# Kernel tuning notes

Measured on AMD Instinct MI355X. Metric: run time of the kernel, lower is better.

## Reference

```python
import jax, jax.numpy as jnp
import numpy as np

D = 32          # max_delay_block
NEG_INF = -1e13 # matches module's self.neg_inf


def setup_inputs() -> dict:
    key = jax.random.key(0)
    ks = jax.random.split(key, 8)
    b, c, t, f, h = 2, 128, 512, 64, 32
    xm = jax.random.normal(ks[0], (b, c, t, f), dtype=jnp.float32)
    xf = jax.random.normal(ks[1], (b, c, t, f), dtype=jnp.float32)
    # pointwise_conv1 / pointwise_conv2: 1x1 convs == per-pixel linear maps c->h
    w1 = jax.random.normal(ks[2], (c, h), dtype=jnp.float32) * (1.0 / np.sqrt(c))
    b1 = jax.random.normal(ks[3], (h,), dtype=jnp.float32) * 0.01
    w2 = jax.random.normal(ks[4], (c, h), dtype=jnp.float32) * (1.0 / np.sqrt(c))
    b2 = jax.random.normal(ks[5], (h,), dtype=jnp.float32) * 0.01
    # conv2d: h -> 1 channels, kernel (5,3)   (OIHW layout)
    wc = jax.random.normal(ks[6], (1, h, 5, 3), dtype=jnp.float32) * (1.0 / np.sqrt(h * 15))
    bc = jax.random.normal(ks[7], (1,), dtype=jnp.float32) * 0.01
    return {"xm": xm, "xf": xf, "w1": w1, "b1": b1, "w2": w2, "b2": b2, "wc": wc, "bc": bc}


def reference(xm, xf, w1, b1, w2, b2, wc, bc):
    b, c, t, f = xf.shape
    # 1x1 convs (per time-freq bin linear projections)
    xm1 = jnp.einsum('bctf,ch->bhtf', xm, w1) + b1[None, :, None, None]
    xf1 = jnp.einsum('bctf,ch->bhtf', xf, w2) + b2[None, :, None, None]

    # delay windows: window j at frame i looks at original frame i + j - (D-1)
    # (j = D-1 is zero delay, j = 0 is delay D-1; out-of-range frames are zero-padded)
    idx = jnp.arange(t)[:, None] + jnp.arange(D)[None, :]          # [t, D] into padded time
    xf1p = jnp.pad(xf1, ((0, 0), (0, 0), (D - 1, 0), (0, 0)))      # [b,h,t+D-1,f]
    win = xf1p[:, :, idx, :]                                       # [b,h,t,D,f]
    corr = jnp.einsum('bhtf,bhtdf->bhtd', xm1, win)                # [b,h,t,D]

    # conv2d smoothing: kernel (5,3), pad (3,1) -> height t+2, keep first t rows
    corr1 = jax.lax.conv_general_dilated(
        corr, wc, window_strides=(1, 1), padding=((3, 3), (1, 1)),
        dimension_numbers=('NCHW', 'OIHW', 'NCHW'))
    corr1 = corr1[:, 0, :t, :] + bc[0]                             # [b,t,D]

    # causal mask: frame i cannot attend to delays pointing before frame 0,
    # i.e. positions with i + j < D - 1 get neg_inf (exactly tril().flip() logic)
    bad = (jnp.arange(t)[:, None] + jnp.arange(D)[None, :]) < (D - 1)
    corr1 = jnp.where(bad[None, :, :], NEG_INF, corr1)
    w = jax.nn.softmax(corr1, axis=-1)                             # [b,t,D]

    # delay-weighted sum over the raw far-end features
    xfp = jnp.pad(xf, ((0, 0), (0, 0), (D - 1, 0), (0, 0)))        # [b,c,t+D-1,f]
    win2 = xfp[:, :, idx, :]                                       # [b,c,t,D,f]
    out = jnp.einsum('btd,bctdf->bctf', w, win2)                   # [b,c,t,f]
    return out
```

## Files before the change

### kernel.cpp

```cpp
#include <hip/hip_runtime.h>

typedef unsigned short u16;
typedef unsigned int   u32;

#define B_ 2
#define C_ 128
#define T_ 512
#define F_ 64
#define H_ 32
#define D_ 32

#define XM1_OUT 0u
#define XF1_OUT 2097152u

#define CORR_OFF 0u
#define CORR_N   1127168u
#define WQ_OFF   1127168u
#define WT_OFF   1159936u
#define FLAG_OFF 1168673u

__device__ __forceinline__ float scrub_u(u32 v){
  return ((v & 0x7F800000u) == 0x7F800000u) ? 0.f : __uint_as_float(v);
}
__device__ __forceinline__ float bf_lo(u32 u){ return scrub_u(u << 16); }
__device__ __forceinline__ float bf_hi(u32 u){ return scrub_u(u & 0xffff0000u); }
__device__ __forceinline__ float bf1(u16 v){ return scrub_u(((u32)v) << 16); }
__device__ __forceinline__ float f32s(float x){ return scrub_u(__float_as_uint(x)); }
__device__ __forceinline__ u16 f2bf(float x){
  u32 u = __float_as_uint(x);
  u32 r = u + 0x7fffu + ((u >> 16) & 1u);
  return (u16)(r >> 16);
}

__global__ __launch_bounds__(256) void kd_detect(const u16* __restrict__ w1, u32* __restrict__ flag){
  __shared__ int cnt;
  if (threadIdx.x == 0) cnt = 0;
  __syncthreads();
  int c = 0;
  for (int i = threadIdx.x * 2; i < 4096; i += 512){
    u32 e = ((u32)w1[i] >> 7) & 0xFFu;
    if (e >= 0xBFu) c++;
  }
  atomicAdd(&cnt, c);
  __syncthreads();
  if (threadIdx.x == 0) flag[0] = (cnt > 16) ? 1u : 0u;
}

__global__ __launch_bounds__(256) void k0_init(const void* __restrict__ w1, const void* __restrict__ b1,
                                               const void* __restrict__ w2, const void* __restrict__ b2,
                                               const void* __restrict__ wc, const void* __restrict__ bc,
                                               float* __restrict__ ws, const u32* __restrict__ flag){
  u32 i = blockIdx.x * 256u + threadIdx.x;
  float* cp = ws + CORR_OFF;
  for (u32 k = i; k < CORR_N; k += gridDim.x * 256u) cp[k] = 0.f;
  float* wt = ws + WT_OFF;
  u32 isf = *flag;
  if (!isf){
    const u16* W1=(const u16*)w1; const u16* B1=(const u16*)b1;
    const u16* W2=(const u16*)w2; const u16* B2=(const u16*)b2;
    const u16* WC=(const u16*)wc; const u16* BC=(const u16*)bc;
    if (i < 4096u) wt[i]        = bf1(W1[i]);
    if (i < 32u)   wt[4096u+i]  = bf1(B1[i]);
    if (i < 4096u) wt[4128u+i]  = bf1(W2[i]);
    if (i < 32u)   wt[8224u+i]  = bf1(B2[i]);
    if (i < 480u)  wt[8256u+i]  = bf1(WC[i]);
    if (i == 0u)   wt[8736u]    = bf1(BC[0]);
  } else {
    const float* W1=(const float*)w1; const float* B1=(const float*)b1;
    const float* W2=(const float*)w2; const float* B2=(const float*)b2;
    const float* WC=(const float*)wc; const float* BC=(const float*)bc;
    if (i < 4096u) wt[i]        = f32s(W1[i]);
    if (i < 32u)   wt[4096u+i]  = f32s(B1[i]);
    if (i < 4096u) wt[4128u+i]  = f32s(W2[i]);
    if (i < 32u)   wt[8224u+i]  = f32s(B2[i]);
    if (i < 480u)  wt[8256u+i]  = f32s(WC[i]);
    if (i == 0u)   wt[8736u]    = f32s(BC[0]);
  }
}

__global__ __launch_bounds__(256) void k1_proj(const void* __restrict__ xm, const void* __restrict__ xf,
                                               const float* __restrict__ wt, const u32* __restrict__ flag,
                                               float* __restrict__ xm1, float* __restrict__ xf1){
  int bt  = blockIdx.x >> 6;
  int b   = bt >> 1, sel = bt & 1;
  int m0  = (((blockIdx.x & 63) << 8) + threadIdx.x) * 2;
  const void* Xv = sel ? xf : xm;
  const float* W = wt + (sel ? 4128 : 0);
  const float* bias = wt + (sel ? 8224 : 4096);
  u32 isf = *flag;

  float acc0[H_], acc1[H_];
#pragma unroll
  for (int h = 0; h < H_; h++){ acc0[h] = 0.f; acc1[h] = 0.f; }

  if (!isf){
    const u16* X = (const u16*)Xv + (size_t)b * (C_*T_*F_);
    for (int c = 0; c < C_; c++){
      u32 u = *(const u32*)(X + (size_t)c * (T_*F_) + m0);
      float x0 = bf_lo(u), x1 = bf_hi(u);
#pragma unroll
      for (int h = 0; h < H_; h++){
        float wv = W[c * H_ + h];
        acc0[h] += x0 * wv;
        acc1[h] += x1 * wv;
      }
    }
  } else {
    const float* X = (const float*)Xv + (size_t)b * (C_*T_*F_);
    for (int c = 0; c < C_; c++){
      float2 xv = *(const float2*)(X + (size_t)c * (T_*F_) + m0);
      float x0 = f32s(xv.x), x1 = f32s(xv.y);
#pragma unroll
      for (int h = 0; h < H_; h++){
        float wv = W[c * H_ + h];
        acc0[h] += x0 * wv;
        acc1[h] += x1 * wv;
      }
    }
  }
  float* O = (sel ? xf1 : xm1) + (size_t)b * (H_*T_*F_);
#pragma unroll
  for (int h = 0; h < H_; h++){
    float bv = bias[h];
    *(float2*)(O + (size_t)h * (T_*F_) + m0) = make_float2(acc0[h] + bv, acc1[h] + bv);
  }
}

__global__ __launch_bounds__(256) void k2_corr(const float* __restrict__ xm1, const float* __restrict__ xf1,
                                               float* __restrict__ corr_pad){
  int blk = blockIdx.x;
  int tt = blk & 7, h = (blk >> 3) & 31, b = blk >> 8;
  int t0 = tt * 64;
  const float* A  = xm1 + ((size_t)(b*H_ + h)) * (T_*F_);
  const float* Bm = xf1 + ((size_t)(b*H_ + h)) * (T_*F_);

  __shared__ float Al[64*68];
  __shared__ float Bl[95*68];
  int tid = threadIdx.x;

  for (int idx = tid; idx < 64*16; idx += 256){
    int r = idx >> 4, q = idx & 15;
    *(float4*)(Al + r*68 + q*4) = *(const float4*)(A + (size_t)(t0 + r)*F_ + q*4);
  }
  for (int idx = tid; idx < 95*16; idx += 256){
    int r = idx >> 4, q = idx & 15;
    int gr = t0 - 31 + r;
    float4 v = make_float4(0.f,0.f,0.f,0.f);
    if (gr >= 0) v = *(const float4*)(Bm + (size_t)gr*F_ + q*4);
    *(float4*)(Bl + r*68 + q*4) = v;
  }
  __syncthreads();

  int tl = tid >> 2, dg = tid & 3;
  float acc[8];
#pragma unroll
  for (int j = 0; j < 8; j++) acc[j] = 0.f;

  for (int fq = 0; fq < 16; fq++){
    float4 a = *(const float4*)(Al + tl*68 + fq*4);
#pragma unroll
    for (int j = 0; j < 8; j++){
      float4 bv = *(const float4*)(Bl + (tl + dg*8 + j)*68 + fq*4);
      acc[j] += a.x*bv.x + a.y*bv.y + a.z*bv.z + a.w*bv.w;
    }
  }
  float* o = corr_pad + ((size_t)(b*H_ + h))*(518*34) + (size_t)(t0 + tl + 3)*34 + (dg*8 + 1);
#pragma unroll
  for (int j = 0; j < 8; j++) o[j] = acc[j];
}

__global__ __launch_bounds__(256) void k3_conv_softmax(const float* __restrict__ corr_pad,
                                                       const float* __restrict__ wt,
                                                       float* __restrict__ wq){
  int b  = blockIdx.x >> 6;
  int t0 = (blockIdx.x & 63) * 8;
  int tid = threadIdx.x;
  int tl = tid >> 5, d = tid & 31;
  int t = t0 + tl;

  const float* wcf = wt + 8256;
  float val = wt[8736];
  const float* cp = corr_pad + (size_t)b * (H_*518*34);

  for (int h = 0; h < H_; h++){
    const float* cph = cp + (size_t)h*(518*34) + (size_t)t*34 + d;
    const float* wch = wcf + h*15;
#pragma unroll
    for (int kh = 0; kh < 5; kh++){
#pragma unroll
      for (int kw = 0; kw < 3; kw++){
        val += cph[kh*34 + kw] * wch[kh*3 + kw];
      }
    }
  }
  if (t + d < D_ - 1) val = -1e13f;

  float m = val;
#pragma unroll
  for (int off = 16; off > 0; off >>= 1) m = fmaxf(m, __shfl_xor(m, off));
  float e = __expf(val - m);
  float s = e;
#pragma unroll
  for (int off = 16; off > 0; off >>= 1) s += __shfl_xor(s, off);

  wq[((size_t)b*T_ + t)*D_ + d] = e / s;
}

__global__ __launch_bounds__(256) void k4_out(const void* __restrict__ xf, const float* __restrict__ wq,
                                              const u32* __restrict__ flag, void* __restrict__ out){
  int blk = blockIdx.x;
  int tt = blk & 7, c = (blk >> 3) & 127, b = blk >> 10;
  int t0 = tt * 64;
  u32 isf = *flag;

  __shared__ float xfl[95*68];
  __shared__ float wl[64*33];
  int tid = threadIdx.x;

  if (!isf){
    const u16* Xf = (const u16*)xf + ((size_t)(b*C_ + c)) * (T_*F_);
    for (int idx = tid; idx < 95*16; idx += 256){
      int r = idx >> 4, q = idx & 15;
      int gr = t0 - 31 + r;
      float4 v = make_float4(0.f,0.f,0.f,0.f);
      if (gr >= 0){
        uint2 u = *(const uint2*)(Xf + (size_t)gr*F_ + q*4);
        v.x = bf_lo(u.x); v.y = bf_hi(u.x); v.z = bf_lo(u.y); v.w = bf_hi(u.y);
      }
      *(float4*)(xfl + r*68 + q*4) = v;
    }
  } else {
    const float* Xf = (const float*)xf + ((size_t)(b*C_ + c)) * (T_*F_);
    for (int idx = tid; idx < 95*16; idx += 256){
      int r = idx >> 4, q = idx & 15;
      int gr = t0 - 31 + r;
      float4 v = make_float4(0.f,0.f,0.f,0.f);
      if (gr >= 0){
        float4 u = *(const float4*)(Xf + (size_t)gr*F_ + q*4);
        v.x = f32s(u.x); v.y = f32s(u.y); v.z = f32s(u.z); v.w = f32s(u.w);
      }
      *(float4*)(xfl + r*68 + q*4) = v;
    }
  }
  for (int idx = tid; idx < 64*8; idx += 256){
    int r = idx >> 3, q = idx & 7;
    float4 v = *(const float4*)(wq + ((size_t)b*T_ + t0 + r)*D_ + q*4);
    wl[r*33 + q*4 + 0] = v.x; wl[r*33 + q*4 + 1] = v.y;
    wl[r*33 + q*4 + 2] = v.z; wl[r*33 + q*4 + 3] = v.w;
  }
  __syncthreads();

  int tg = tid >> 4, q = tid & 15;
  float4 acc[4];
#pragma unroll
  for (int j = 0; j < 4; j++) acc[j] = make_float4(0.f,0.f,0.f,0.f);

#pragma unroll
  for (int rr = 0; rr < 35; rr++){
    float4 xv = *(const float4*)(xfl + (tg*4 + rr)*68 + q*4);
#pragma unroll
    for (int j = 0; j < 4; j++){
      int d = rr - j;
      if (d >= 0 && d < D_){
        float wv = wl[(tg*4 + j)*33 + d];
        acc[j].x += wv * xv.x; acc[j].y += wv * xv.y;
        acc[j].z += wv * xv.z; acc[j].w += wv * xv.w;
      }
    }
  }
  if (!isf){
#pragma unroll
    for (int j = 0; j < 4; j++){
      int t = t0 + tg*4 + j;
      u16* O = (u16*)out + (((size_t)(b*C_ + c))*T_ + t)*F_ + q*4;
      u32 lo = (u32)f2bf(acc[j].x) | ((u32)f2bf(acc[j].y) << 16);
      u32 hi = (u32)f2bf(acc[j].z) | ((u32)f2bf(acc[j].w) << 16);
      *(uint2*)O = make_uint2(lo, hi);
    }
  } else {
#pragma unroll
    for (int j = 0; j < 4; j++){
      int t = t0 + tg*4 + j;
      float* O = (float*)out + (((size_t)(b*C_ + c))*T_ + t)*F_ + q*4;
      *(float4*)O = acc[j];
    }
  }
}

extern "C" void kernel_launch(void* const* d_in, const int* in_sizes, int n_in,
                              void* d_out, int out_size, void* d_ws, size_t ws_size,
                              hipStream_t stream) {
  const void* xm = d_in[0];
  const void* xf = d_in[1];
  float* ws = (float*)d_ws;
  u32* flag = (u32*)(ws + FLAG_OFF);

  float* xm1 = (float*)d_out + XM1_OUT;
  float* xf1 = (float*)d_out + XF1_OUT;

  hipLaunchKernelGGL(kd_detect, dim3(1), dim3(256), 0, stream, (const u16*)d_in[2], flag);
  hipLaunchKernelGGL(k0_init, dim3(1024), dim3(256), 0, stream, d_in[2], d_in[3], d_in[4],
                     d_in[5], d_in[6], d_in[7], ws, flag);
  hipLaunchKernelGGL(k1_proj, dim3(256), dim3(256), 0, stream, xm, xf, ws + WT_OFF, flag, xm1, xf1);
  hipLaunchKernelGGL(k2_corr, dim3(512), dim3(256), 0, stream, xm1, xf1, ws + CORR_OFF);
  hipLaunchKernelGGL(k3_conv_softmax, dim3(128), dim3(256), 0, stream, ws + CORR_OFF,
                     ws + WT_OFF, ws + WQ_OFF);
  hipLaunchKernelGGL(k4_out, dim3(2048), dim3(256), 0, stream, xf, ws + WQ_OFF, flag, d_out);
}
```

Baseline: 200.1 us.

## Drop dtype detection and weight-staging kernels, stage inputs through shared memory

Result: faster. 188.0 us (-6.0%).

```diff
diff --git a/kernel.cpp b/kernel.cpp
--- a/kernel.cpp
+++ b/kernel.cpp
@@ -14,116 +14,49 @@
 #define XF1_OUT 2097152u
 
 #define CORR_OFF 0u
-#define CORR_N   1127168u
 #define WQ_OFF   1127168u
-#define WT_OFF   1159936u
-#define FLAG_OFF 1168673u
-
-__device__ __forceinline__ float scrub_u(u32 v){
-  return ((v & 0x7F800000u) == 0x7F800000u) ? 0.f : __uint_as_float(v);
-}
-__device__ __forceinline__ float bf_lo(u32 u){ return scrub_u(u << 16); }
-__device__ __forceinline__ float bf_hi(u32 u){ return scrub_u(u & 0xffff0000u); }
-__device__ __forceinline__ float bf1(u16 v){ return scrub_u(((u32)v) << 16); }
-__device__ __forceinline__ float f32s(float x){ return scrub_u(__float_as_uint(x)); }
-__device__ __forceinline__ u16 f2bf(float x){
-  u32 u = __float_as_uint(x);
-  u32 r = u + 0x7fffu + ((u >> 16) & 1u);
-  return (u16)(r >> 16);
-}
-
-__global__ __launch_bounds__(256) void kd_detect(const u16* __restrict__ w1, u32* __restrict__ flag){
-  __shared__ int cnt;
-  if (threadIdx.x == 0) cnt = 0;
-  __syncthreads();
-  int c = 0;
-  for (int i = threadIdx.x * 2; i < 4096; i += 512){
-    u32 e = ((u32)w1[i] >> 7) & 0xFFu;
-    if (e >= 0xBFu) c++;
-  }
-  atomicAdd(&cnt, c);
-  __syncthreads();
-  if (threadIdx.x == 0) flag[0] = (cnt > 16) ? 1u : 0u;
-}
-
-__global__ __launch_bounds__(256) void k0_init(const void* __restrict__ w1, const void* __restrict__ b1,
-                                               const void* __restrict__ w2, const void* __restrict__ b2,
-                                               const void* __restrict__ wc, const void* __restrict__ bc,
-                                               float* __restrict__ ws, const u32* __restrict__ flag){
-  u32 i = blockIdx.x * 256u + threadIdx.x;
-  float* cp = ws + CORR_OFF;
-  for (u32 k = i; k < CORR_N; k += gridDim.x * 256u) cp[k] = 0.f;
-  float* wt = ws + WT_OFF;
-  u32 isf = *flag;
-  if (!isf){
-    const u16* W1=(const u16*)w1; const u16* B1=(const u16*)b1;
-    const u16* W2=(const u16*)w2; const u16* B2=(const u16*)b2;
-    const u16* WC=(const u16*)wc; const u16* BC=(const u16*)bc;
-    if (i < 4096u) wt[i]        = bf1(W1[i]);
-    if (i < 32u)   wt[4096u+i]  = bf1(B1[i]);
-    if (i < 4096u) wt[4128u+i]  = bf1(W2[i]);
-    if (i < 32u)   wt[8224u+i]  = bf1(B2[i]);
-    if (i < 480u)  wt[8256u+i]  = bf1(WC[i]);
-    if (i == 0u)   wt[8736u]    = bf1(BC[0]);
-  } else {
-    const float* W1=(const float*)w1; const float* B1=(const float*)b1;
-    const float* W2=(const float*)w2; const float* B2=(const float*)b2;
-    const float* WC=(const float*)wc; const float* BC=(const float*)bc;
-    if (i < 4096u) wt[i]        = f32s(W1[i]);
-    if (i < 32u)   wt[4096u+i]  = f32s(B1[i]);
-    if (i < 4096u) wt[4128u+i]  = f32s(W2[i]);
-    if (i < 32u)   wt[8224u+i]  = f32s(B2[i]);
-    if (i < 480u)  wt[8256u+i]  = f32s(WC[i]);
-    if (i == 0u)   wt[8736u]    = f32s(BC[0]);
-  }
-}
-
-__global__ __launch_bounds__(256) void k1_proj(const void* __restrict__ xm, const void* __restrict__ xf,
-                                               const float* __restrict__ wt, const u32* __restrict__ flag,
+
+__global__ __launch_bounds__(256) void k1_proj(const float* __restrict__ xm, const float* __restrict__ xf,
+                                               const float* __restrict__ w1, const float* __restrict__ b1,
+                                               const float* __restrict__ w2, const float* __restrict__ b2,
                                                float* __restrict__ xm1, float* __restrict__ xf1){
-  int bt  = blockIdx.x >> 6;
-  int b   = bt >> 1, sel = bt & 1;
-  int m0  = (((blockIdx.x & 63) << 8) + threadIdx.x) * 2;
-  const void* Xv = sel ? xf : xm;
-  const float* W = wt + (sel ? 4128 : 0);
-  const float* bias = wt + (sel ? 8224 : 4096);
-  u32 isf = *flag;
-
-  float acc0[H_], acc1[H_];
-#pragma unroll
-  for (int h = 0; h < H_; h++){ acc0[h] = 0.f; acc1[h] = 0.f; }
-
-  if (!isf){
-    const u16* X = (const u16*)Xv + (size_t)b * (C_*T_*F_);
-    for (int c = 0; c < C_; c++){
-      u32 u = *(const u32*)(X + (size_t)c * (T_*F_) + m0);
-      float x0 = bf_lo(u), x1 = bf_hi(u);
-#pragma unroll
-      for (int h = 0; h < H_; h++){
-        float wv = W[c * H_ + h];
-        acc0[h] += x0 * wv;
-        acc1[h] += x1 * wv;
-      }
-    }
-  } else {
-    const float* X = (const float*)Xv + (size_t)b * (C_*T_*F_);
-    for (int c = 0; c < C_; c++){
-      float2 xv = *(const float2*)(X + (size_t)c * (T_*F_) + m0);
-      float x0 = f32s(xv.x), x1 = f32s(xv.y);
-#pragma unroll
-      for (int h = 0; h < H_; h++){
-        float wv = W[c * H_ + h];
-        acc0[h] += x0 * wv;
-        acc1[h] += x1 * wv;
-      }
-    }
-  }
-  float* O = (sel ? xf1 : xm1) + (size_t)b * (H_*T_*F_);
-#pragma unroll
-  for (int h = 0; h < H_; h++){
-    float bv = bias[h];
-    *(float2*)(O + (size_t)h * (T_*F_) + m0) = make_float2(acc0[h] + bv, acc1[h] + bv);
-  }
+  int blk  = blockIdx.x;
+  int mblk = blk & 127;
+  int bt   = blk >> 7;
+  int b    = bt >> 1, sel = bt & 1;
+  int tid  = threadIdx.x;
+  int m0   = mblk * 256;
+
+  const float* X    = (sel ? xf : xm) + (size_t)b * (C_*T_*F_);
+  const float* W    = sel ? w2 : w1;
+  const float* bias = sel ? b2 : b1;
+
+  __shared__ float ls[32*256];
+
+  float acc[H_];
+#pragma unroll
+  for (int h = 0; h < H_; h++) acc[h] = 0.f;
+
+  for (int cc = 0; cc < C_; cc += 32){
+    for (int idx = tid; idx < 32*64; idx += 256){
+      int r = idx >> 6, q = idx & 63;
+      *(float4*)(ls + r*256 + q*4) =
+        *(const float4*)(X + (size_t)(cc + r) * (T_*F_) + m0 + q*4);
+    }
+    __syncthreads();
+#pragma unroll
+    for (int r = 0; r < 32; r++){
+      float x = ls[r*256 + tid];
+      const float* Wr = W + (cc + r) * H_;
+#pragma unroll
+      for (int h = 0; h < H_; h++) acc[h] += x * Wr[h];
+    }
+    __syncthreads();
+  }
+
+  float* O = (sel ? xf1 : xm1) + (size_t)b * (H_*T_*F_) + m0 + tid;
+#pragma unroll
+  for (int h = 0; h < H_; h++) O[(size_t)h * (T_*F_)] = acc[h] + bias[h];
 }
 
 __global__ __launch_bounds__(256) void k2_corr(const float* __restrict__ xm1, const float* __restrict__ xf1,
@@ -170,26 +103,35 @@
 }
 
 __global__ __launch_bounds__(256) void k3_conv_softmax(const float* __restrict__ corr_pad,
-                                                       const float* __restrict__ wt,
+                                                       const float* __restrict__ wc, const float* __restrict__ bc,
                                                        float* __restrict__ wq){
   int b  = blockIdx.x >> 6;
   int t0 = (blockIdx.x & 63) * 8;
   int tid = threadIdx.x;
+
+  __shared__ float ls[32*12*34];
+  const float* cp = corr_pad + (size_t)b * (H_*518*34);
+  for (int idx = tid; idx < 32*12*34; idx += 256){
+    int h = idx / 408, rem = idx - h*408;
+    int r = rem / 34, dd = rem - r*34;
+    int gr = t0 + r;
+    bool halo = (gr < 3) | (gr > 514) | (dd == 0) | (dd == 33);
+    ls[idx] = halo ? 0.f : cp[(size_t)h*(518*34) + (size_t)gr*34 + dd];
+  }
+  __syncthreads();
+
   int tl = tid >> 5, d = tid & 31;
   int t = t0 + tl;
 
-  const float* wcf = wt + 8256;
-  float val = wt[8736];
-  const float* cp = corr_pad + (size_t)b * (H_*518*34);
-
+  float val = bc[0];
   for (int h = 0; h < H_; h++){
-    const float* cph = cp + (size_t)h*(518*34) + (size_t)t*34 + d;
-    const float* wch = wcf + h*15;
+    const float* base = ls + h*408 + tl*34 + d;
+    const float* wch = wc + h*15;
 #pragma unroll
     for (int kh = 0; kh < 5; kh++){
 #pragma unroll
       for (int kw = 0; kw < 3; kw++){
-        val += cph[kh*34 + kw] * wch[kh*3 + kw];
+        val += base[kh*34 + kw] * wch[kh*3 + kw];
       }
     }
   }
@@ -206,41 +148,23 @@
   wq[((size_t)b*T_ + t)*D_ + d] = e / s;
 }
 
-__global__ __launch_bounds__(256) void k4_out(const void* __restrict__ xf, const float* __restrict__ wq,
-                                              const u32* __restrict__ flag, void* __restrict__ out){
+__global__ __launch_bounds__(256) void k4_out(const float* __restrict__ xf, const float* __restrict__ wq,
+                                              float* __restrict__ out){
   int blk = blockIdx.x;
   int tt = blk & 7, c = (blk >> 3) & 127, b = blk >> 10;
   int t0 = tt * 64;
-  u32 isf = *flag;
+  const float* Xf = xf + ((size_t)(b*C_ + c)) * (T_*F_);
 
   __shared__ float xfl[95*68];
   __shared__ float wl[64*33];
   int tid = threadIdx.x;
 
-  if (!isf){
-    const u16* Xf = (const u16*)xf + ((size_t)(b*C_ + c)) * (T_*F_);
-    for (int idx = tid; idx < 95*16; idx += 256){
-      int r = idx >> 4, q = idx & 15;
-      int gr = t0 - 31 + r;
-      float4 v = make_float4(0.f,0.f,0.f,0.f);
-      if (gr >= 0){
-        uint2 u = *(const uint2*)(Xf + (size_t)gr*F_ + q*4);
-        v.x = bf_lo(u.x); v.y = bf_hi(u.x); v.z = bf_lo(u.y); v.w = bf_hi(u.y);
-      }
-      *(float4*)(xfl + r*68 + q*4) = v;
-    }
-  } else {
-    const float* Xf = (const float*)xf + ((size_t)(b*C_ + c)) * (T_*F_);
-    for (int idx = tid; idx < 95*16; idx += 256){
-      int r = idx >> 4, q = idx & 15;
-      int gr = t0 - 31 + r;
-      float4 v = make_float4(0.f,0.f,0.f,0.f);
-      if (gr >= 0){
-        float4 u = *(const float4*)(Xf + (size_t)gr*F_ + q*4);
-        v.x = f32s(u.x); v.y = f32s(u.y); v.z = f32s(u.z); v.w = f32s(u.w);
-      }
-      *(float4*)(xfl + r*68 + q*4) = v;
-    }
+  for (int idx = tid; idx < 95*16; idx += 256){
+    int r = idx >> 4, q = idx & 15;
+    int gr = t0 - 31 + r;
+    float4 v = make_float4(0.f,0.f,0.f,0.f);
+    if (gr >= 0) v = *(const float4*)(Xf + (size_t)gr*F_ + q*4);
+    *(float4*)(xfl + r*68 + q*4) = v;
   }
   for (int idx = tid; idx < 64*8; idx += 256){
     int r = idx >> 3, q = idx & 7;
@@ -268,42 +192,32 @@
       }
     }
   }
-  if (!isf){
-#pragma unroll
-    for (int j = 0; j < 4; j++){
-      int t = t0 + tg*4 + j;
-      u16* O = (u16*)out + (((size_t)(b*C_ + c))*T_ + t)*F_ + q*4;
-      u32 lo = (u32)f2bf(acc[j].x) | ((u32)f2bf(acc[j].y) << 16);
-      u32 hi = (u32)f2bf(acc[j].z) | ((u32)f2bf(acc[j].w) << 16);
-      *(uint2*)O = make_uint2(lo, hi);
-    }
-  } else {
-#pragma unroll
-    for (int j = 0; j < 4; j++){
-      int t = t0 + tg*4 + j;
-      float* O = (float*)out + (((size_t)(b*C_ + c))*T_ + t)*F_ + q*4;
-      *(float4*)O = acc[j];
-    }
+#pragma unroll
+  for (int j = 0; j < 4; j++){
+    int t = t0 + tg*4 + j;
+    float* O = out + (((size_t)(b*C_ + c))*T_ + t)*F_ + q*4;
+    *(float4*)O = acc[j];
   }
 }
 
 extern "C" void kernel_launch(void* const* d_in, const int* in_sizes, int n_in,
                               void* d_out, int out_size, void* d_ws, size_t ws_size,
                               hipStream_t stream) {
-  const void* xm = d_in[0];
-  const void* xf = d_in[1];
+  const float* xm = (const float*)d_in[0];
+  const float* xf = (const float*)d_in[1];
+  const float* w1 = (const float*)d_in[2];
+  const float* b1 = (const float*)d_in[3];
+  const float* w2 = (const float*)d_in[4];
+  const float* b2 = (const float*)d_in[5];
+  const float* wc = (const float*)d_in[6];
+  const float* bc = (const float*)d_in[7];
   float* ws = (float*)d_ws;
-  u32* flag = (u32*)(ws + FLAG_OFF);
 
   float* xm1 = (float*)d_out + XM1_OUT;
   float* xf1 = (float*)d_out + XF1_OUT;
 
-  hipLaunchKernelGGL(kd_detect, dim3(1), dim3(256), 0, stream, (const u16*)d_in[2], flag);
-  hipLaunchKernelGGL(k0_init, dim3(1024), dim3(256), 0, stream, d_in[2], d_in[3], d_in[4],
-                     d_in[5], d_in[6], d_in[7], ws, flag);
-  hipLaunchKernelGGL(k1_proj, dim3(256), dim3(256), 0, stream, xm, xf, ws + WT_OFF, flag, xm1, xf1);
+  hipLaunchKernelGGL(k1_proj, dim3(512), dim3(256), 0, stream, xm, xf, w1, b1, w2, b2, xm1, xf1);
   hipLaunchKernelGGL(k2_corr, dim3(512), dim3(256), 0, stream, xm1, xf1, ws + CORR_OFF);
-  hipLaunchKernelGGL(k3_conv_softmax, dim3(128), dim3(256), 0, stream, ws + CORR_OFF,
-                     ws + WT_OFF, ws + WQ_OFF);
-  hipLaunchKernelGGL(k4_out, dim3(2048), dim3(256), 0, stream, xf, ws + WQ_OFF, flag, d_out);
-}
+  hipLaunchKernelGGL(k3_conv_softmax, dim3(128), dim3(256), 0, stream, ws + CORR_OFF, wc, bc, ws + WQ_OFF);
+  hipLaunchKernelGGL(k4_out, dim3(2048), dim3(256), 0, stream, xf, ws + WQ_OFF, (float*)d_out);
+}
```
